# Performance work log

Hardware: AMD Instinct MI355X
Metric: run time of the kernel (lower is better)

## Reference

```python
import jax, jax.numpy as jnp
import numpy as np

DIM_MODEL = 1024
NUM_HEADS = 16
HEAD_DIM = DIM_MODEL // NUM_HEADS
NEG_INF = -1e9


def setup_inputs() -> dict:
    key = jax.random.key(0)
    ks = jax.random.split(key, 12)
    B, S = 4, 2048
    s = 1.0 / np.sqrt(DIM_MODEL)
    inp = {
        "query": jax.random.normal(ks[0], (B, S, DIM_MODEL), jnp.float32),
        "key": jax.random.normal(ks[1], (B, S, DIM_MODEL), jnp.float32),
        "value": jax.random.normal(ks[2], (B, S, DIM_MODEL), jnp.float32),
        "mask": jax.random.randint(ks[3], (B, 1, S, S), 0, 2, jnp.int32),
        "Wq": jax.random.normal(ks[4], (DIM_MODEL, DIM_MODEL), jnp.float32) * s,
        "bq": jnp.zeros((DIM_MODEL,), jnp.float32),
        "Wk": jax.random.normal(ks[5], (DIM_MODEL, DIM_MODEL), jnp.float32) * s,
        "bk": jnp.zeros((DIM_MODEL,), jnp.float32),
        "Wv": jax.random.normal(ks[6], (DIM_MODEL, DIM_MODEL), jnp.float32) * s,
        "bv": jnp.zeros((DIM_MODEL,), jnp.float32),
        "Wo": jax.random.normal(ks[7], (DIM_MODEL, DIM_MODEL), jnp.float32) * s,
        "bo": jnp.zeros((DIM_MODEL,), jnp.float32),
    }
    return inp


def _split_heads(x, B):
    # [B, S, D] -> [B, H, S, Dh]
    S = x.shape[1]
    return x.reshape(B, S, NUM_HEADS, HEAD_DIM).transpose(0, 2, 1, 3)


def reference(query, key, value, mask, Wq, bq, Wk, bk, Wv, bv, Wo, bo):
    B = query.shape[0]
    q = _split_heads(query @ Wq + bq, B)   # [B,H,Sq,Dh]
    k = _split_heads(key @ Wk + bk, B)     # [B,H,Sk,Dh]
    v = _split_heads(value @ Wv + bv, B)   # [B,H,Sk,Dh]

    scale = 1.0 / np.sqrt(HEAD_DIM)
    scores = jnp.einsum("bhqd,bhkd->bhqk", q, k) * scale  # [B,H,Sq,Sk]
    scores = jnp.where(mask == 0, NEG_INF, scores)
    probs = jax.nn.softmax(scores, axis=-1)
    attn = jnp.einsum("bhqk,bhkd->bhqd", probs, v)         # [B,H,Sq,Dh]

    attn = attn.transpose(0, 2, 1, 3).reshape(B, -1, DIM_MODEL)  # [B,Sq,D]
    return attn @ Wo + bo
```

## Files before the change

kernel.cpp:

```cpp
#include <hip/hip_runtime.h>


typedef unsigned short u16;
typedef _Float16 f16;
typedef __attribute__((ext_vector_type(8))) _Float16 half8;
typedef __attribute__((ext_vector_type(8))) unsigned short u16x8;
typedef __attribute__((ext_vector_type(4))) unsigned short u16x4;
typedef __attribute__((ext_vector_type(4))) float floatx4;

__device__ f16 g_Bt[4][1024 * 1024];
__device__ f16 g_X[3][8192 * 1024];
__device__ f16 g_Qh[8192 * 1024];
__device__ f16 g_Kh[8192 * 1024];
__device__ f16 g_Vh[8192 * 1024];
__device__ f16 g_Vt[(size_t)4 * 16 * 64 * 2048];
__device__ f16 g_Oh[8192 * 1024];
__device__ u16 g_pbias[(size_t)4 * 2048 * 2048];
__device__ int g_is_bf16;

__device__ __forceinline__ float bf2f(u16 u) {
  union { unsigned int i; float f; } v;
  v.i = ((unsigned int)u) << 16;
  return v.f;
}
__device__ __forceinline__ u16 f2h_bits(float f) {
  union { _Float16 h; u16 u; } v;
  v.h = (_Float16)f;
  return v.u;
}

__global__ void detect_kernel(const u16* __restrict__ q) {
  if (threadIdx.x == 0) {
    int cnt = 0;
    for (int i = 0; i < 256; ++i) {
      const u16 v = q[i];
      const int e = (v >> 7) & 0xFF;
      cnt += ((e >= 100 && e <= 135) || ((v & 0x7FFF) == 0)) ? 1 : 0;
    }
    g_is_bf16 = (cnt >= 205) ? 1 : 0;
  }
}

__device__ __forceinline__ float load_in(const void* p, size_t i) {
  return g_is_bf16 ? bf2f(((const u16*)p)[i]) : ((const float*)p)[i];
}

__device__ __forceinline__ int swz128(int row, int cb) {
  return row * 128 + (cb ^ ((row & 7) << 4));
}
__device__ __forceinline__ int swz(int row, int cb) {
  return ((row << 6) + cb) ^ ((row & 7) << 4);
}

__device__ __forceinline__ void gl_lds16(void* g, void* l) {
  __builtin_amdgcn_global_load_lds(
      (__attribute__((address_space(1))) void*)g,
      (__attribute__((address_space(3))) void*)l, 16, 0, 0);
}

__global__ __launch_bounds__(256) void cvt_kernel(
    const void* __restrict__ q, const void* __restrict__ k,
    const void* __restrict__ v) {
  const int z = blockIdx.y;
  const void* x = (z == 0) ? q : (z == 1) ? k : v;
  f16* oh = g_X[z];
  const size_t i = ((size_t)blockIdx.x * 256 + threadIdx.x) * 8;
  half8 h;
  if (!g_is_bf16) {
    const float* xf = (const float*)x + i;
    const float4 a = *(const float4*)xf;
    const float4 b = *(const float4*)(xf + 4);
    h[0] = (f16)a.x; h[1] = (f16)a.y; h[2] = (f16)a.z; h[3] = (f16)a.w;
    h[4] = (f16)b.x; h[5] = (f16)b.y; h[6] = (f16)b.z; h[7] = (f16)b.w;
  } else {
    const u16x8 a = *(const u16x8*)((const u16*)x + i);
#pragma unroll
    for (int j = 0; j < 8; ++j) h[j] = (f16)bf2f(a[j]);
  }
  *(half8*)(oh + i) = h;
}

__global__ __launch_bounds__(256) void maskbias_kernel(const int* __restrict__ mask) {
  const size_t tid = (size_t)blockIdx.x * 256 + threadIdx.x;
  const size_t base = tid * 4;
  const int b = (int)(base >> 22);
  const size_t rem = base & 0x3FFFFFu;
  const int row = (int)(rem >> 11);
  const int c0 = (int)(rem & 2047);
  const int4 m = *(const int4*)(mask + base);
  const int tile = c0 >> 6;
  const int cl = c0 & 63;
  const int lan = cl & 15;
  const int ni = cl >> 4;
  u16* dst = g_pbias + ((size_t)b << 22) + ((size_t)row << 11) + tile * 64 + ni;
  const u16 NEG = 0xCE6E;
  dst[(lan + 0) * 4] = m.x ? (u16)0 : NEG;
  dst[(lan + 1) * 4] = m.y ? (u16)0 : NEG;
  dst[(lan + 2) * 4] = m.z ? (u16)0 : NEG;
  dst[(lan + 3) * 4] = m.w ? (u16)0 : NEG;
}

__global__ void wtrans_kernel(const void* __restrict__ Wq,
                              const void* __restrict__ Wk,
                              const void* __restrict__ Wv,
                              const void* __restrict__ Wo) {
  __shared__ float tile[32][33];
  const int wo = blockIdx.z;
  const void* in = (wo == 0) ? Wq : (wo == 1) ? Wk : (wo == 2) ? Wv : Wo;
  const int tx = threadIdx.x, ty = threadIdx.y;
  const int n0 = blockIdx.x * 32, k0 = blockIdx.y * 32;
  tile[ty][tx] = load_in(in, (size_t)(k0 + ty) * 1024 + n0 + tx);
  __syncthreads();
  g_Bt[wo][(size_t)(n0 + ty) * 1024 + k0 + tx] = (f16)tile[tx][ty];
}

__global__ __launch_bounds__(512) void vtrans_kernel() {
  __shared__ f16 tile[64][65];
  const int tx = threadIdx.x, ty = threadIdx.y;
  const int t0 = blockIdx.x * 64;
  const int h = blockIdx.y;
  const int b = blockIdx.z;
#pragma unroll
  for (int i = 0; i < 8; ++i) {
    const int row = ty + i * 8;
    tile[row][tx] = g_Vh[(size_t)(b * 2048 + t0 + row) * 1024 + h * 64 + tx];
  }
  __syncthreads();
#pragma unroll
  for (int i = 0; i < 8; ++i) {
    const int d = ty + i * 8;
    g_Vt[((size_t)(b * 16 + h) * 64 + d) * 2048 + t0 + tx] = tile[tx][d];
  }
}

#define GEMM_CORE(AP, BP)                                                    \
  const int t = threadIdx.x;                                                 \
  const int lane = t & 63;                                                   \
  const int lanelo = lane & 15;                                              \
  const int quad = lane >> 4;                                                \
  const int wave = t >> 6;                                                   \
  const int wr = wave >> 1, wc = wave & 1;                                   \
  const int bm = blockIdx.x * 128;                                           \
  const int bn = blockIdx.y * 128;                                           \
         \
  const int s4 = lane << 4;                                                  \
  const int rl = s4 ^ ((s4 >> 2) & 0x70) ^ ((s4 >> 4) & 0x10);               \
  const int r0 = wave * 16 + (rl >> 6);            \
  const int cbb = rl & 63;                             \
  const char* pA0 = (const char*)(AP) + (size_t)(bm + r0) * 2048 + cbb;      \
  const char* pA1 = pA0 + (size_t)64 * 2048;                                 \
  const char* pB0 = (const char*)(BP) + (size_t)(bn + r0) * 2048 + cbb;      \
  const char* pB1 = pB0 + (size_t)64 * 2048;                                 \
  u16* lA0 = &As[wave * 512]; u16* lA1 = &As[2048 + wave * 512];             \
  u16* lB0 = &Bs[wave * 512]; u16* lB1 = &Bs[2048 + wave * 512];             \
  floatx4 acc[4][4];                                                         \
  _Pragma("unroll") for (int i = 0; i < 4; ++i)                              \
      _Pragma("unroll") for (int j = 0; j < 4; ++j) acc[i][j] = (floatx4)(0.f); \
  for (int k0 = 0; k0 < 1024; k0 += 32) {                                    \
    __syncthreads();                              \
    const size_t kb = (size_t)(k0 << 1);                                     \
    gl_lds16((void*)(pA0 + kb), lA0);                                        \
    gl_lds16((void*)(pA1 + kb), lA1);                                        \
    gl_lds16((void*)(pB0 + kb), lB0);                                        \
    gl_lds16((void*)(pB1 + kb), lB1);                                        \
    __syncthreads();       \
    half8 af[4], bf_[4];                                                     \
    _Pragma("unroll") for (int mi = 0; mi < 4; ++mi) {                       \
      const int row = wr * 64 + mi * 16 + lanelo;                            \
      af[mi] = *(const half8*)&As[swz(row, quad * 16) >> 1];                 \
    }                                                                        \
    _Pragma("unroll") for (int ni = 0; ni < 4; ++ni) {                       \
      const int row = wc * 64 + ni * 16 + lanelo;                            \
      bf_[ni] = *(const half8*)&Bs[swz(row, quad * 16) >> 1];                \
    }                                                                        \
    _Pragma("unroll") for (int mi = 0; mi < 4; ++mi)                         \
        _Pragma("unroll") for (int ni = 0; ni < 4; ++ni)                     \
      acc[mi][ni] = __builtin_amdgcn_mfma_f32_16x16x32_f16(                  \
          af[mi], bf_[ni], acc[mi][ni], 0, 0, 0);                            \
  }

__global__ __launch_bounds__(256) void gemm_qkv_kernel(
    const void* __restrict__ bq, const void* __restrict__ bk,
    const void* __restrict__ bv) {
  __shared__ __align__(16) u16 As[4096];
  __shared__ __align__(16) u16 Bs[4096];
  const int z = blockIdx.z;
  const void* bias = (z == 0) ? bq : (z == 1) ? bk : bv;
  f16* Ch = (z == 0) ? g_Qh : (z == 1) ? g_Kh : g_Vh;

  GEMM_CORE(g_X[z], g_Bt[z])

  const float sc_ = (z == 0) ? 0.125f : 1.0f;
#pragma unroll
  for (int ni = 0; ni < 4; ++ni) {
    const int col = bn + wc * 64 + ni * 16 + lanelo;
    const float bvv = load_in(bias, col);
#pragma unroll
    for (int mi = 0; mi < 4; ++mi) {
#pragma unroll
      for (int rg = 0; rg < 4; ++rg) {
        const int row = bm + wr * 64 + mi * 16 + quad * 4 + rg;
        Ch[(size_t)row * 1024 + col] = (f16)((acc[mi][ni][rg] + bvv) * sc_);
      }
    }
  }
}

__global__ __launch_bounds__(256) void gemm_o_kernel(
    const void* __restrict__ bias, float* __restrict__ Cptr) {
  __shared__ __align__(16) u16 As[4096];
  __shared__ __align__(16) u16 Bs[4096];

  GEMM_CORE(g_Oh, g_Bt[3])

#pragma unroll
  for (int ni = 0; ni < 4; ++ni) {
    const int col = bn + wc * 64 + ni * 16 + lanelo;
    const float bvv = load_in(bias, col);
#pragma unroll
    for (int mi = 0; mi < 4; ++mi) {
#pragma unroll
      for (int rg = 0; rg < 4; ++rg) {
        const int row = bm + wr * 64 + mi * 16 + quad * 4 + rg;
        Cptr[(size_t)row * 1024 + col] = acc[mi][ni][rg] + bvv;
      }
    }
  }
}

__global__ __launch_bounds__(512, 4) void attn_mfma_kernel() {
  constexpr int S = 2048, D = 1024, NT = S / 64;
  __shared__ __align__(16) u16 k_s[64 * 64];
  __shared__ __align__(16) u16 vt_s[64 * 64];
  __shared__ __align__(16) u16 p_s[256 * 64];

  const int t = threadIdx.x;
  const int lane = t & 63;
  const int lanelo = lane & 15;
  const int quad = lane >> 4;
  const int wave = t >> 6;

  const int q0 = blockIdx.x * 256;
  const int h = blockIdx.y;
  const int b = blockIdx.z;
  const size_t bh = (size_t)b * S * D + (size_t)h * 64;

  half8 a_q[2][2];
#pragma unroll
  for (int g = 0; g < 2; ++g)
#pragma unroll
    for (int kk = 0; kk < 2; ++kk)
      a_q[g][kk] = *(const half8*)(g_Qh + bh +
          (size_t)(q0 + wave * 32 + g * 16 + lanelo) * D + kk * 32 + quad * 8);

  half8 b_ones;
#pragma unroll
  for (int j = 0; j < 8; ++j)
    b_ones[j] = (lanelo == 0) ? (f16)1.0f : (f16)0.0f;

  const int sj = t & 63;
  const int scc = (t >> 6) * 8;
  const int koff = swz128(sj, scc * 2) >> 1;

  const u16* Kbase = (const u16*)g_Kh + bh + (size_t)sj * D + scc;
  const u16* Vbase = (const u16*)g_Vt +
                     ((size_t)(b * 16 + h) * 64 + sj) * 2048 + scc;
  u16x8 kreg = *(const u16x8*)(Kbase);
  u16x8 vreg = *(const u16x8*)(Vbase);

  floatx4 o_acc[2][4];
#pragma unroll
  for (int g = 0; g < 2; ++g)
#pragma unroll
    for (int ni = 0; ni < 4; ++ni) o_acc[g][ni] = (floatx4)(0.f);
  floatx4 o_l[2] = {(floatx4)(0.f), (floatx4)(0.f)};

  const u16* pbrow = g_pbias + ((size_t)b << 22) +
                     ((size_t)(q0 + wave * 32 + quad * 4) << 11) + (lanelo << 2);

  for (int kt = 0; kt < NT; ++kt) {
    const int j0 = kt * 64;
    __syncthreads();

    *(u16x8*)&k_s[koff] = kreg;
    *(u16x8*)&vt_s[koff] = vreg;
    __syncthreads();

    {
      const int ktn = (kt + 1 < NT) ? kt + 1 : kt;
      kreg = *(const u16x8*)(Kbase + (size_t)ktn * 64 * D);
      vreg = *(const u16x8*)(Vbase + (size_t)ktn * 64);
    }
    u16x4 bs[2][4];
#pragma unroll
    for (int g = 0; g < 2; ++g)
#pragma unroll
      for (int r = 0; r < 4; ++r)
        bs[g][r] = *(const u16x4*)(pbrow + ((size_t)(g * 16 + r) << 11) + j0);

    floatx4 sacc[2][4];
#pragma unroll
    for (int g = 0; g < 2; ++g)
#pragma unroll
      for (int ni = 0; ni < 4; ++ni)
#pragma unroll
        for (int r = 0; r < 4; ++r) sacc[g][ni][r] = bf2f(bs[g][r][ni]);
#pragma unroll
    for (int kk = 0; kk < 2; ++kk) {
#pragma unroll
      for (int ni = 0; ni < 4; ++ni) {
        const half8 bb = *(const half8*)
            &k_s[swz128(ni * 16 + lanelo, kk * 64 + quad * 16) >> 1];
#pragma unroll
        for (int g = 0; g < 2; ++g)
          sacc[g][ni] = __builtin_amdgcn_mfma_f32_16x16x32_f16(
              a_q[g][kk], bb, sacc[g][ni], 0, 0, 0);
      }
    }

#pragma unroll
    for (int g = 0; g < 2; ++g)
#pragma unroll
      for (int r = 0; r < 4; ++r) {
        const int prow = wave * 32 + g * 16 + quad * 4 + r;
#pragma unroll
        for (int ni = 0; ni < 4; ++ni) {
          p_s[swz128(prow, (ni * 16 + lanelo) * 2) >> 1] =
              f2h_bits(__expf(sacc[g][ni][r]));
        }
      }
    asm volatile("s_waitcnt lgkmcnt(0)" ::: "memory");
    __builtin_amdgcn_sched_barrier(0);

#pragma unroll
    for (int kk = 0; kk < 2; ++kk) {
      half8 a_p[2];
#pragma unroll
      for (int g = 0; g < 2; ++g)
        a_p[g] = *(const half8*)
            &p_s[swz128(wave * 32 + g * 16 + lanelo, kk * 64 + quad * 16) >> 1];
#pragma unroll
      for (int ni = 0; ni < 4; ++ni) {
        const half8 bb = *(const half8*)
            &vt_s[swz128(ni * 16 + lanelo, kk * 64 + quad * 16) >> 1];
#pragma unroll
        for (int g = 0; g < 2; ++g)
          o_acc[g][ni] = __builtin_amdgcn_mfma_f32_16x16x32_f16(
              a_p[g], bb, o_acc[g][ni], 0, 0, 0);
      }
#pragma unroll
      for (int g = 0; g < 2; ++g)
        o_l[g] = __builtin_amdgcn_mfma_f32_16x16x32_f16(
            a_p[g], b_ones, o_l[g], 0, 0, 0);
    }
  }

#pragma unroll
  for (int g = 0; g < 2; ++g)
#pragma unroll
    for (int r = 0; r < 4; ++r) {
      const float lsum = __shfl(o_l[g][r], lane & 48);
      const float inv = 1.f / lsum;
      const int row = q0 + wave * 32 + g * 16 + quad * 4 + r;
#pragma unroll
      for (int ni = 0; ni < 4; ++ni)
        g_Oh[bh + (size_t)row * D + ni * 16 + lanelo] =
            (f16)(o_acc[g][ni][r] * inv);
    }
}

extern "C" void kernel_launch(void* const* d_in, const int* in_sizes, int n_in,
                              void* d_out, int out_size, void* d_ws, size_t ws_size,
                              hipStream_t stream) {
  const void* query = d_in[0];
  const void* key   = d_in[1];
  const void* value = d_in[2];
  const int* mask   = (const int*)d_in[3];
  const void* Wq = d_in[4];
  const void* bq = d_in[5];
  const void* Wk = d_in[6];
  const void* bk = d_in[7];
  const void* Wv = d_in[8];
  const void* bv = d_in[9];
  const void* Wo = d_in[10];
  const void* bo = d_in[11];

  detect_kernel<<<1, 64, 0, stream>>>((const u16*)query);

  maskbias_kernel<<<16384, 256, 0, stream>>>(mask);

  wtrans_kernel<<<dim3(32, 32, 4), dim3(32, 32), 0, stream>>>(Wq, Wk, Wv, Wo);

  cvt_kernel<<<dim3(4096, 3), 256, 0, stream>>>(query, key, value);

  gemm_qkv_kernel<<<dim3(64, 8, 3), 256, 0, stream>>>(bq, bk, bv);

  vtrans_kernel<<<dim3(32, 16, 4), dim3(64, 8), 0, stream>>>();

  attn_mfma_kernel<<<dim3(8, 16, 4), 512, 0, stream>>>();

  gemm_o_kernel<<<dim3(64, 8), 256, 0, stream>>>(bo, (float*)d_out);
}
```

Baseline: 634.8 us.

## Use 128-query attention blocks and fold log2e into Q scale for exp2

The attention kernel moves from 512-thread blocks covering 256 queries to 256-thread blocks covering 128 queries. The grid doubles, and each thread now stages two K/V chunks into shared memory instead of one. Separately, log2(e) is folded into the Q scaling and into the mask bias constant so the softmax can call exp2f directly instead of __expf. This aims to improve occupancy and CU load balance and to trim exponent work. The cost is that each K/V tile is now loaded by twice as many blocks, which raises global and L2 traffic.

```diff
diff --git a/kernel.cpp b/kernel.cpp
--- a/kernel.cpp
+++ b/kernel.cpp
@@ -93,7 +93,7 @@
   const int lan = cl & 15;
   const int ni = cl >> 4;
   u16* dst = g_pbias + ((size_t)b << 22) + ((size_t)row << 11) + tile * 64 + ni;
-  const u16 NEG = 0xCE6E;
+  const u16 NEG = 0xCEAC;
   dst[(lan + 0) * 4] = m.x ? (u16)0 : NEG;
   dst[(lan + 1) * 4] = m.y ? (u16)0 : NEG;
   dst[(lan + 2) * 4] = m.z ? (u16)0 : NEG;
@@ -190,7 +190,7 @@
 
   GEMM_CORE(g_X[z], g_Bt[z])
 
-  const float sc_ = (z == 0) ? 0.125f : 1.0f;
+  const float sc_ = (z == 0) ? 0.125f * 1.44269504f : 1.0f;
 #pragma unroll
   for (int ni = 0; ni < 4; ++ni) {
     const int col = bn + wc * 64 + ni * 16 + lanelo;
@@ -228,11 +228,11 @@
   }
 }
 
-__global__ __launch_bounds__(512, 4) void attn_mfma_kernel() {
+__global__ __launch_bounds__(256, 4) void attn_mfma_kernel() {
   constexpr int S = 2048, D = 1024, NT = S / 64;
   __shared__ __align__(16) u16 k_s[64 * 64];
   __shared__ __align__(16) u16 vt_s[64 * 64];
-  __shared__ __align__(16) u16 p_s[256 * 64];
+  __shared__ __align__(16) u16 p_s[128 * 64];
 
   const int t = threadIdx.x;
   const int lane = t & 63;
@@ -240,7 +240,7 @@
   const int quad = lane >> 4;
   const int wave = t >> 6;
 
-  const int q0 = blockIdx.x * 256;
+  const int q0 = blockIdx.x * 128;
   const int h = blockIdx.y;
   const int b = blockIdx.z;
   const size_t bh = (size_t)b * S * D + (size_t)h * 64;
@@ -259,14 +259,20 @@
     b_ones[j] = (lanelo == 0) ? (f16)1.0f : (f16)0.0f;
 
   const int sj = t & 63;
-  const int scc = (t >> 6) * 8;
-  const int koff = swz128(sj, scc * 2) >> 1;
-
-  const u16* Kbase = (const u16*)g_Kh + bh + (size_t)sj * D + scc;
+  const int sc0 = (t >> 6) * 8;
+  int koff[2];
+#pragma unroll
+  for (int s = 0; s < 2; ++s) koff[s] = swz128(sj, (sc0 + s * 32) * 2) >> 1;
+
+  const u16* Kbase = (const u16*)g_Kh + bh + (size_t)sj * D + sc0;
   const u16* Vbase = (const u16*)g_Vt +
-                     ((size_t)(b * 16 + h) * 64 + sj) * 2048 + scc;
-  u16x8 kreg = *(const u16x8*)(Kbase);
-  u16x8 vreg = *(const u16x8*)(Vbase);
+                     ((size_t)(b * 16 + h) * 64 + sj) * 2048 + sc0;
+  u16x8 kreg[2], vreg[2];
+#pragma unroll
+  for (int s = 0; s < 2; ++s) {
+    kreg[s] = *(const u16x8*)(Kbase + s * 32);
+    vreg[s] = *(const u16x8*)(Vbase + s * 32);
+  }
 
   floatx4 o_acc[2][4];
 #pragma unroll
@@ -282,14 +288,20 @@
     const int j0 = kt * 64;
     __syncthreads();
 
-    *(u16x8*)&k_s[koff] = kreg;
-    *(u16x8*)&vt_s[koff] = vreg;
+#pragma unroll
+    for (int s = 0; s < 2; ++s) {
+      *(u16x8*)&k_s[koff[s]] = kreg[s];
+      *(u16x8*)&vt_s[koff[s]] = vreg[s];
+    }
     __syncthreads();
 
     {
       const int ktn = (kt + 1 < NT) ? kt + 1 : kt;
-      kreg = *(const u16x8*)(Kbase + (size_t)ktn * 64 * D);
-      vreg = *(const u16x8*)(Vbase + (size_t)ktn * 64);
+#pragma unroll
+      for (int s = 0; s < 2; ++s) {
+        kreg[s] = *(const u16x8*)(Kbase + (size_t)ktn * 64 * D + s * 32);
+        vreg[s] = *(const u16x8*)(Vbase + (size_t)ktn * 64 + s * 32);
+      }
     }
     u16x4 bs[2][4];
 #pragma unroll
@@ -326,7 +338,7 @@
 #pragma unroll
         for (int ni = 0; ni < 4; ++ni) {
           p_s[swz128(prow, (ni * 16 + lanelo) * 2) >> 1] =
-              f2h_bits(__expf(sacc[g][ni][r]));
+              f2h_bits(exp2f(sacc[g][ni][r]));
         }
       }
     asm volatile("s_waitcnt lgkmcnt(0)" ::: "memory");
@@ -397,7 +409,7 @@
 
   vtrans_kernel<<<dim3(32, 16, 4), dim3(64, 8), 0, stream>>>();
 
-  attn_mfma_kernel<<<dim3(8, 16, 4), 512, 0, stream>>>();
+  attn_mfma_kernel<<<dim3(16, 16, 4), 256, 0, stream>>>();
 
   gemm_o_kernel<<<dim3(64, 8), 256, 0, stream>>>(bo, (float*)d_out);
 }
```

Result: slower. 843.3 us (+32.8%).
